# Kernel tuning notes

Measured on AMD Instinct MI355X. Metric: run time of the kernel, lower is better.

The kernel has to match this reference:

```python
import jax, jax.numpy as jnp
import numpy as np

C = 1024
D = C // 8      # query/key channels
R = C // 16     # channel-attention reduction
B, H, W = 4, 64, 64


def setup_inputs() -> dict:
    key = jax.random.key(0)
    ks = jax.random.split(key, 10)
    s = lambda k, shp, fan: jax.random.normal(k, shp, jnp.float32) * (1.0 / np.sqrt(fan))
    return {
        "x": jax.random.normal(ks[0], (B, C, H, W), jnp.float32),
        "x1": jax.random.normal(ks[1], (B, C, H, W), jnp.float32),
        "Wq": s(ks[2], (D, C), C), "bq": jnp.zeros((D,), jnp.float32),
        "Wk": s(ks[3], (D, C), C), "bk": jnp.zeros((D,), jnp.float32),
        "Wv": s(ks[4], (C, C), C), "bv": jnp.zeros((C,), jnp.float32),
        "Wca1": s(ks[5], (R, C), C),  # CBAM MLP, no bias
        "Wca2": s(ks[6], (C, R), R),
    }


def _forward(x, x1, Wq, bq, Wk, bk, Wv, bv, Wca1, Wca2):
    b, c, h, w = x.shape
    n = h * w
    # 1x1 convs as channel matmuls
    Q = (jnp.einsum('bchw,dc->bdhw', x, Wq) + bq[:, None, None]).reshape(b, D, n)   # [B,D,N]
    K = (jnp.einsum('bchw,dc->bdhw', x, Wk) + bk[:, None, None]).reshape(b, D, n)   # [B,D,N]
    V = (jnp.einsum('bchw,oc->bohw', x1, Wv) + bv[:, None, None]).reshape(b, c, n)  # [B,C,N]
    # energy[b,n,m] = Q[:,n] . K[:,m]
    energy = jnp.einsum('bdn,bdm->bnm', Q, K)
    att = jax.nn.sigmoid(energy)                       # [B,N,N]
    # torch: bmm(V, att^T) -> out[b,c,n] = sum_m V[b,c,m] * att[b,n,m]
    out = jnp.einsum('bcm,bnm->bcn', V, att).reshape(b, c, h, w)
    # ChannelAttention (CBAM): shared MLP on avg+max pooled features, sigmoid gate
    avg = out.mean(axis=(2, 3))                        # [B,C]
    mx = out.max(axis=(2, 3))                          # [B,C]
    mlp = lambda v: jnp.einsum('cr,br->bc', Wca2, jax.nn.relu(jnp.einsum('rc,bc->br', Wca1, v)))
    gate = jax.nn.sigmoid(mlp(avg) + mlp(mx))          # [B,C]
    return out * gate[:, :, None, None]


def reference(x, x1, Wq, bq, Wk, bk, Wv, bv, Wca1, Wca2):
    return _forward(x, x1, Wq, bq, Wk, bk, Wv, bv, Wca1, Wca2)
```

## Files before the change

### kernel.cpp

```cpp
#include <hip/hip_runtime.h>
#include <hip/hip_fp16.h>
#include <cstdint>

typedef _Float16 f16;
typedef __attribute__((ext_vector_type(8))) _Float16 half8;
typedef __attribute__((ext_vector_type(16))) float floatx16;

#define CC 1024
#define DD 128
#define RRR 64
#define BBATCH 4
#define NNN 4096

#define BM 128
#define BN 128
#define BK 64

__device__ __forceinline__ void gl_lds16(const void* g, void* l) {
  __builtin_amdgcn_global_load_lds(
      (__attribute__((address_space(1))) void*)(uintptr_t)g,
      (__attribute__((address_space(3))) void*)l, 16, 0, 0);
}

template<int EPI>
__global__ __launch_bounds__(256)
void gemm_bt(const f16* __restrict__ A, const f16* __restrict__ Bp, f16* __restrict__ Cout,
             const float* __restrict__ bias, int N, int K,
             int lda, int ldb, int ldc, size_t sA, size_t sB, size_t sC)
{
  __shared__ __align__(16) f16 S[2 * BM * BK];
  f16* As = S;
  f16* Bs = S + BM * BK;

  const int z = blockIdx.z;
  const int tid  = threadIdx.x;
  const int lane = tid & 63;
  const int wave = tid >> 6;
  const int m0 = blockIdx.y * BM;
  const int n0 = blockIdx.x * BN;
  const int wm = (wave >> 1) * 64;
  const int wn = (wave & 1) * 64;
  const int l31 = lane & 31;
  const int hi  = lane >> 5;
  const int rs  = lane & 7;

  const f16* Ab = A  + (size_t)z * sA + (size_t)m0 * lda;
  const f16* Bb = Bp + (size_t)z * sB + (size_t)n0 * ldb;

  floatx16 acc[2][2];
#pragma unroll
  for (int i = 0; i < 2; ++i)
#pragma unroll
    for (int j = 0; j < 2; ++j)
#pragma unroll
      for (int r = 0; r < 16; ++r)
        acc[i][j][r] = 0.f;

  int srow[4], ssrc[4];
#pragma unroll
  for (int r = 0; r < 4; ++r) {
    const int gi = r * 256 + tid;
    const int row = gi >> 3;
    const int gc  = gi & 7;
    srow[r] = row;
    ssrc[r] = ((gc ^ (row & 7)) << 3);
  }

  for (int k0 = 0; k0 < K; k0 += BK) {
#pragma unroll
    for (int r = 0; r < 4; ++r) {
      gl_lds16(Ab + (size_t)srow[r] * lda + k0 + ssrc[r], As + (size_t)(r * 256 + tid) * 8);
      gl_lds16(Bb + (size_t)srow[r] * ldb + k0 + ssrc[r], Bs + (size_t)(r * 256 + tid) * 8);
    }
    __syncthreads();

#pragma unroll
    for (int kk = 0; kk < BK; kk += 16) {
      const int gr = (((kk >> 3) + hi) ^ rs) << 3;
      half8 af[2], bfr[2];
#pragma unroll
      for (int i = 0; i < 2; ++i)
        af[i] = *(const half8*)(As + (wm + i * 32 + l31) * BK + gr);
#pragma unroll
      for (int j = 0; j < 2; ++j)
        bfr[j] = *(const half8*)(Bs + (wn + j * 32 + l31) * BK + gr);
#pragma unroll
      for (int i = 0; i < 2; ++i)
#pragma unroll
        for (int j = 0; j < 2; ++j)
          acc[i][j] = __builtin_amdgcn_mfma_f32_32x32x16_f16(af[i], bfr[j], acc[i][j], 0, 0, 0);
    }
    __syncthreads();
  }

  f16* Ch = Cout + (size_t)z * sC;
  f16* Ct = S;
#pragma unroll
  for (int i = 0; i < 2; ++i)
#pragma unroll
    for (int j = 0; j < 2; ++j)
#pragma unroll
      for (int r = 0; r < 16; ++r) {
        const int rl = wm + i * 32 + (r & 3) + 8 * (r >> 2) + 4 * hi;
        const int cl = wn + j * 32 + l31;
        const float v = acc[i][j][r];
        f16 h;
        if constexpr (EPI == 0)      h = (f16)v;
        else if constexpr (EPI == 1) h = (f16)(v + bias[m0 + rl]);
        else if constexpr (EPI == 2) h = (f16)(v + bias[n0 + cl]);
        else                         h = (f16)(1.0f / (1.0f + __expf(-v)));
        Ct[rl * BN + ((((cl >> 3) ^ (rl & 7)) << 3) | (cl & 7))] = h;
      }
  __syncthreads();
#pragma unroll
  for (int p = 0; p < 8; ++p) {
    const int idx = p * 256 + tid;
    const int rl = idx >> 4;
    const int g  = idx & 15;
    half8 vv = *(const half8*)(Ct + rl * BN + ((g ^ (rl & 7)) << 3));
    *(half8*)(Ch + (size_t)(m0 + rl) * ldc + n0 + g * 8) = vv;
  }
}

#define G8_STAGE(MATG, MIDX, LD, H, KT, BUF) do {                                   \
    gl_lds16(MATG + (size_t)((H) * 128 + srow) * (LD) + (KT) * 64 + soff,           \
             &S[BUF][MIDX][(H) * 8192 + tid * 8]);                                  \
    gl_lds16(MATG + (size_t)((H) * 128 + 64 + srow) * (LD) + (KT) * 64 + soff,      \
             &S[BUF][MIDX][(H) * 8192 + 4096 + tid * 8]);                           \
  } while (0)

#define G8_LOADA(QM) do {                                                           \
    _Pragma("unroll") for (int mt = 0; mt < 2; ++mt)                                \
    _Pragma("unroll") for (int ks = 0; ks < 4; ++ks)                                \
      af[mt * 4 + ks] = *(const half8*)(Ac + aRow + ((QM) * 2 + mt) * 2048 + sws[ks]); \
  } while (0)

#define G8_LOADB(NT2) do {                                                          \
    _Pragma("unroll") for (int ks = 0; ks < 4; ++ks)                                \
      bf[(NT2) * 4 + ks] = *(const half8*)(Bc + bRow + (NT2) * 2048 + sws[ks]);     \
  } while (0)

#define G8_MFMA(QM, QN) do {                                                        \
    __builtin_amdgcn_s_setprio(1);                                                  \
    _Pragma("unroll") for (int mt = 0; mt < 2; ++mt)                                \
    _Pragma("unroll") for (int ks = 0; ks < 4; ++ks)                                \
      acc[(QM) * 2 + mt][QN] = __builtin_amdgcn_mfma_f32_32x32x16_f16(              \
          af[mt * 4 + ks], bf[(QN) * 4 + ks], acc[(QM) * 2 + mt][QN], 0, 0, 0);     \
    __builtin_amdgcn_s_setprio(0);                                                  \
  } while (0)

template<int EPI>
__global__ __launch_bounds__(512, 2)
void gemm8p(const f16* __restrict__ A, const f16* __restrict__ Bp, f16* __restrict__ Cout,
            const float* __restrict__ bias, int K,
            int lda, int ldb, int ldc, size_t sA, size_t sB, size_t sC)
{
  __shared__ __align__(16) f16 S[2][2][16384];

  const int tid  = threadIdx.x;
  const int lane = tid & 63;
  const int wave = tid >> 6;
  const int wm   = wave >> 2;
  const int wn   = wave & 3;
  const int l31  = lane & 31;
  const int hi   = lane >> 5;
  const int z    = blockIdx.z;
  const int m0   = blockIdx.y * 256;
  const int n0   = blockIdx.x * 256;

  const f16* Ag = A  + (size_t)z * sA + (size_t)m0 * lda;
  const f16* Bg = Bp + (size_t)z * sB + (size_t)n0 * ldb;

  const int srow = tid >> 3;
  const int soff = (((tid & 7) ^ (srow & 7)) << 3);

  int sws[4];
#pragma unroll
  for (int ks = 0; ks < 4; ++ks) sws[ks] = (((ks * 2 + hi) ^ (l31 & 7)) << 3);
  const int aRow = (wm * 128 + l31) * 64;
  const int bRow = (wn * 64 + l31) * 64;

  floatx16 acc[4][2];
#pragma unroll
  for (int i = 0; i < 4; ++i)
#pragma unroll
    for (int j = 0; j < 2; ++j)
#pragma unroll
      for (int r = 0; r < 16; ++r) acc[i][j][r] = 0.f;

  half8 af[8], bf[8];

  G8_STAGE(Ag, 0, lda, 0, 0, 0);
  G8_STAGE(Bg, 1, ldb, 0, 0, 0);
  G8_STAGE(Ag, 0, lda, 1, 0, 0);
  G8_STAGE(Bg, 1, ldb, 1, 0, 0);

  const int NT = K >> 6;
  for (int t = 0; t < NT; ++t) {
    const int cur = t & 1, nxt = cur ^ 1;
    const f16* Ac = &S[cur][0][0];
    const f16* Bc = &S[cur][1][0];
    const bool pf = (t + 1 < NT);

    if (pf) {
      G8_STAGE(Ag, 0, lda, 0, t + 1, nxt);
      G8_STAGE(Bg, 1, ldb, 0, t + 1, nxt);
      asm volatile("s_waitcnt vmcnt(4)" ::: "memory");
    } else {
      asm volatile("s_waitcnt vmcnt(0)" ::: "memory");
    }
    __builtin_amdgcn_s_barrier();
    G8_LOADA(0); G8_LOADB(0);
    asm volatile("s_waitcnt lgkmcnt(0)" ::: "memory");
    __builtin_amdgcn_sched_barrier(0);
    G8_MFMA(0, 0);
    __builtin_amdgcn_s_barrier();

    G8_LOADB(1);
    if (pf) G8_STAGE(Ag, 0, lda, 1, t + 1, nxt);
    __builtin_amdgcn_s_barrier();
    asm volatile("s_waitcnt lgkmcnt(0)" ::: "memory");
    __builtin_amdgcn_sched_barrier(0);
    G8_MFMA(0, 1);
    __builtin_amdgcn_s_barrier();

    G8_LOADA(1);
    if (pf) G8_STAGE(Bg, 1, ldb, 1, t + 1, nxt);
    __builtin_amdgcn_s_barrier();
    asm volatile("s_waitcnt lgkmcnt(0)" ::: "memory");
    __builtin_amdgcn_sched_barrier(0);
    G8_MFMA(1, 1);
    __builtin_amdgcn_s_barrier();

    G8_MFMA(1, 0);
    __builtin_amdgcn_s_barrier();
  }

  f16* Ct = &S[0][0][0];
  f16* Ch = Cout + (size_t)z * sC;
#pragma unroll
  for (int i = 0; i < 4; ++i)
#pragma unroll
    for (int j = 0; j < 2; ++j)
#pragma unroll
      for (int r = 0; r < 16; ++r) {
        const int rl = wm * 128 + i * 32 + (r & 3) + 8 * (r >> 2) + 4 * hi;
        const int cl = wn * 64 + j * 32 + l31;
        const float v = acc[i][j][r];
        f16 h;
        if constexpr (EPI == 1) h = (f16)(v + bias[m0 + rl]);
        else                    h = (f16)v;
        Ct[rl * 256 + ((((cl >> 3) ^ (rl & 7)) << 3) | (cl & 7))] = h;
      }
  asm volatile("s_waitcnt lgkmcnt(0)" ::: "memory");
  __builtin_amdgcn_s_barrier();
#pragma unroll
  for (int p = 0; p < 16; ++p) {
    const int idx = p * 512 + tid;
    const int rl = idx >> 5;
    const int g  = idx & 31;
    half8 vv = *(const half8*)(Ct + rl * 256 + ((g ^ (rl & 7)) << 3));
    *(half8*)(Ch + (size_t)(m0 + rl) * ldc + n0 + g * 8) = vv;
  }
}

#undef G8_STAGE
#undef G8_LOADA
#undef G8_LOADB
#undef G8_MFMA

__global__ __launch_bounds__(256)
void prep(const float* __restrict__ Wq, const float* __restrict__ Wk, const float* __restrict__ Wv,
          const float* __restrict__ bq, const float* __restrict__ bk,
          f16* __restrict__ WQKb, f16* __restrict__ Wvb, float* __restrict__ bqk)
{
  const int NV = CC * CC;
  const int NQ = DD * CC;
  int i = blockIdx.x * 256 + threadIdx.x;
  if (i < NV)                    Wvb[i] = (f16)Wv[i];
  else if (i < NV + NQ)          WQKb[i - NV] = (f16)Wq[i - NV];
  else if (i < NV + 2 * NQ)      WQKb[i - NV] = (f16)Wk[i - NV - NQ];
  else if (i < NV + 2 * NQ + 2 * DD) {
    int t = i - NV - 2 * NQ;
    bqk[t] = (t < DD) ? bq[t] : bk[t - DD];
  }
}

__global__ __launch_bounds__(256)
void transpose_cvt(const float* __restrict__ x, const float* __restrict__ x1,
                   f16* __restrict__ ox, f16* __restrict__ ox1, int nb)
{
  const int zz = blockIdx.z;
  const int b  = (zz < nb) ? zz : zz - nb;
  const float* in = ((zz < nb) ? x : x1) + (size_t)b * CC * NNN;
  f16* out = ((zz < nb) ? ox : ox1) + (size_t)b * CC * NNN;
  __shared__ float tile[64][65];
  const int c0 = blockIdx.y * 64;
  const int n0 = blockIdx.x * 64;
  const int t  = threadIdx.x;
  const int rn = (t & 15) * 4;
  const int rc = t >> 4;
#pragma unroll
  for (int r = 0; r < 4; ++r) {
    const float4 v = *(const float4*)(in + (size_t)(c0 + rc + r * 16) * NNN + n0 + rn);
    tile[rc + r * 16][rn]     = v.x;
    tile[rc + r * 16][rn + 1] = v.y;
    tile[rc + r * 16][rn + 2] = v.z;
    tile[rc + r * 16][rn + 3] = v.w;
  }
  __syncthreads();
  const int ce = (t & 7) * 8;
  const int nr = t >> 3;
#pragma unroll
  for (int r = 0; r < 2; ++r) {
    half8 vv;
#pragma unroll
    for (int e = 0; e < 8; ++e) vv[e] = (f16)tile[ce + e][nr + r * 32];
    *(half8*)(out + (size_t)(n0 + nr + r * 32) * CC + c0 + ce) = vv;
  }
}

__global__ __launch_bounds__(256)
void rowreduce(const f16* __restrict__ X, float* __restrict__ avg, float* __restrict__ mx, int ncols)
{
  const size_t ridx = (size_t)blockIdx.y * gridDim.x + blockIdx.x;
  const half8* p = (const half8*)(X + ridx * ncols);
  float s = 0.f, m = -3.402823466e38f;
  for (int i = threadIdx.x; i < ncols / 8; i += 256) {
    half8 v = p[i];
#pragma unroll
    for (int e = 0; e < 8; ++e) {
      float f = (float)v[e];
      s += f;
      m = fmaxf(m, f);
    }
  }
#pragma unroll
  for (int o = 32; o > 0; o >>= 1) {
    s += __shfl_down(s, o);
    m = fmaxf(m, __shfl_down(m, o));
  }
  __shared__ float ss[4], sm[4];
  if ((threadIdx.x & 63) == 0) { ss[threadIdx.x >> 6] = s; sm[threadIdx.x >> 6] = m; }
  __syncthreads();
  if (threadIdx.x == 0) {
    s = ss[0] + ss[1] + ss[2] + ss[3];
    m = fmaxf(fmaxf(sm[0], sm[1]), fmaxf(sm[2], sm[3]));
    avg[ridx] = s / (float)ncols;
    mx[ridx] = m;
  }
}

__global__ __launch_bounds__(256)
void mlp_gate(const float* __restrict__ avg, const float* __restrict__ mxv,
              const float* __restrict__ W1, const float* __restrict__ W2,
              float* __restrict__ gate)
{
  const int z = blockIdx.x;
  avg += (size_t)z * CC; mxv += (size_t)z * CC; gate += (size_t)z * CC;
  const int t = threadIdx.x;
  const int r = t & 63;
  const int part = t >> 6;
  __shared__ float pa[4][64], pm[4][64], h[RRR];
  {
    const float* w = W1 + (size_t)r * CC + part * 256;
    const float* av = avg + part * 256;
    const float* mv = mxv + part * 256;
    float sa = 0.f, sm = 0.f;
    for (int c = 0; c < 256; ++c) { float wv = w[c]; sa += wv * av[c]; sm += wv * mv[c]; }
    pa[part][r] = sa; pm[part][r] = sm;
  }
  __syncthreads();
  if (t < RRR) {
    float A_ = pa[0][t] + pa[1][t] + pa[2][t] + pa[3][t];
    float M_ = pm[0][t] + pm[1][t] + pm[2][t] + pm[3][t];
    h[t] = fmaxf(A_, 0.f) + fmaxf(M_, 0.f);
  }
  __syncthreads();
  for (int c = t; c < CC; c += 256) {
    float s = 0.f;
    for (int rr = 0; rr < RRR; ++rr) s += W2[(size_t)c * RRR + rr] * h[rr];
    gate[c] = 1.0f / (1.0f + __expf(-s));
  }
}

__global__ __launch_bounds__(256)
void scale_out(const f16* __restrict__ oh, float* __restrict__ out, const float* __restrict__ gate)
{
  oh  += (size_t)blockIdx.y * CC * NNN;
  out += (size_t)blockIdx.y * CC * NNN;
  gate += (size_t)blockIdx.y * CC;
  size_t i = (size_t)blockIdx.x * 256 + threadIdx.x;
  half8 v = ((const half8*)oh)[i];
  const float g = gate[(i * 8) >> 12];
  float4 a = { (float)v[0] * g, (float)v[1] * g, (float)v[2] * g, (float)v[3] * g };
  float4 b = { (float)v[4] * g, (float)v[5] * g, (float)v[6] * g, (float)v[7] * g };
  float4* o = (float4*)out;
  o[2 * i]     = a;
  o[2 * i + 1] = b;
}

extern "C" void kernel_launch(void* const* d_in, const int* in_sizes, int n_in,
                              void* d_out, int out_size, void* d_ws, size_t ws_size,
                              hipStream_t stream)
{
  const float* x    = (const float*)d_in[0];
  const float* x1   = (const float*)d_in[1];
  const float* Wq   = (const float*)d_in[2];
  const float* bq   = (const float*)d_in[3];
  const float* Wk   = (const float*)d_in[4];
  const float* bk   = (const float*)d_in[5];
  const float* Wv   = (const float*)d_in[6];
  const float* bv   = (const float*)d_in[7];
  const float* Wca1 = (const float*)d_in[8];
  const float* Wca2 = (const float*)d_in[9];
  float* out = (float*)d_out;

  char* ws = (char*)d_ws;
  size_t off = 0;
  auto alloc = [&](size_t bytes) { void* p = ws + off; off += (bytes + 255) & ~255ULL; return p; };

  f16* WQKb = (f16*)alloc((size_t)2 * DD * CC * 2);
  f16* Wvb  = (f16*)alloc((size_t)CC * CC * 2);
  float* bqk  = (float*)alloc(256 * 4);
  float* avg  = (float*)alloc((size_t)BBATCH * CC * 4);
  float* mxv  = (float*)alloc((size_t)BBATCH * CC * 4);
  float* gate = (float*)alloc((size_t)BBATCH * CC * 4);

  const size_t attB = (size_t)NNN * NNN * 2;
  const size_t xTB  = (size_t)BBATCH * NNN * CC * 2;
  const size_t qkB  = (size_t)BBATCH * NNN * 2 * DD * 2;
  const size_t vBB  = (size_t)BBATCH * CC * NNN * 2;
  const size_t ohB  = (size_t)BBATCH * CC * NNN * 2;
  const size_t fixedEnd = off;

  const dim3 blk(256);
  const int prepN = CC * CC + 2 * DD * CC + 2 * DD;
  prep<<<(prepN + 255) / 256, blk, 0, stream>>>(Wq, Wk, Wv, bq, bk, WQKb, Wvb, bqk);

  {
    size_t offF = fixedEnd;
    auto af_ = [&](size_t bytes) { void* p = ws + offF; offF += (bytes + 255) & ~255ULL; return p; };
    f16* QKt  = (f16*)af_(qkB);
    f16* Vb   = (f16*)af_(vBB);
    f16* outh = (f16*)af_(ohB);
    f16* att  = (f16*)af_((size_t)BBATCH * attB);
    if (offF + (1 << 20) <= ws_size) {
      f16* xTb  = att;
      f16* x1Tb = att + (size_t)BBATCH * NNN * CC;

      transpose_cvt<<<dim3(NNN / 64, CC / 64, 2 * BBATCH), blk, 0, stream>>>(x, x1, xTb, x1Tb, BBATCH);

      gemm_bt<2><<<dim3(2 * DD / BN, NNN / BM, BBATCH), blk, 0, stream>>>(
          xTb, WQKb, QKt, bqk, 2 * DD, CC,
          CC, CC, 2 * DD, (size_t)NNN * CC, 0, (size_t)NNN * 2 * DD);
      gemm8p<1><<<dim3(NNN / 256, CC / 256, BBATCH), dim3(512), 0, stream>>>(
          Wvb, x1Tb, Vb, bv, CC,
          CC, CC, NNN, 0, (size_t)NNN * CC, (size_t)CC * NNN);

      const size_t sQK = (size_t)NNN * 2 * DD;
      gemm_bt<3><<<dim3(NNN / BN, NNN / BM, BBATCH), blk, 0, stream>>>(
          QKt, QKt + DD, att, nullptr, NNN, DD,
          2 * DD, 2 * DD, NNN, sQK, sQK, (size_t)NNN * NNN);
      gemm8p<0><<<dim3(NNN / 256, CC / 256, BBATCH), dim3(512), 0, stream>>>(
          Vb, att, outh, nullptr, NNN,
          NNN, NNN, NNN, (size_t)CC * NNN, (size_t)NNN * NNN, (size_t)CC * NNN);

      rowreduce<<<dim3(CC, BBATCH), blk, 0, stream>>>(outh, avg, mxv, NNN);
      mlp_gate<<<BBATCH, blk, 0, stream>>>(avg, mxv, Wca1, Wca2, gate);
      scale_out<<<dim3(CC * NNN / 8 / 256, BBATCH), blk, 0, stream>>>(outh, out, gate);
      return;
    }
  }

  int g = 0;
  for (int cand = BBATCH; cand >= 1; cand >>= 1) {
    size_t need = fixedEnd + 2 * xTB + qkB + vBB + ohB + (size_t)cand * attB + (1 << 20);
    if (need <= ws_size) { g = cand; break; }
  }

  if (g > 0) {
    f16* xTb  = (f16*)alloc(xTB);
    f16* x1Tb = (f16*)alloc(xTB);
    f16* QKt  = (f16*)alloc(qkB);
    f16* Vb   = (f16*)alloc(vBB);
    f16* outh = (f16*)alloc(ohB);
    f16* att  = (f16*)alloc((size_t)g * attB);

    transpose_cvt<<<dim3(NNN / 64, CC / 64, 2 * BBATCH), blk, 0, stream>>>(x, x1, xTb, x1Tb, BBATCH);

    gemm_bt<2><<<dim3(2 * DD / BN, NNN / BM, BBATCH), blk, 0, stream>>>(
        xTb, WQKb, QKt, bqk, 2 * DD, CC,
        CC, CC, 2 * DD, (size_t)NNN * CC, 0, (size_t)NNN * 2 * DD);
    gemm_bt<1><<<dim3(NNN / BN, CC / BM, BBATCH), blk, 0, stream>>>(
        Wvb, x1Tb, Vb, bv, NNN, CC,
        CC, CC, NNN, 0, (size_t)NNN * CC, (size_t)CC * NNN);

    for (int b0 = 0; b0 < BBATCH; b0 += g) {
      const int gc = (b0 + g <= BBATCH) ? g : (BBATCH - b0);
      const size_t sQK = (size_t)NNN * 2 * DD;
      gemm_bt<3><<<dim3(NNN / BN, NNN / BM, gc), blk, 0, stream>>>(
          QKt + (size_t)b0 * sQK, QKt + (size_t)b0 * sQK + DD, att, nullptr,
          NNN, DD, 2 * DD, 2 * DD, NNN, sQK, sQK, (size_t)NNN * NNN);
      gemm_bt<0><<<dim3(NNN / BN, CC / BM, gc), blk, 0, stream>>>(
          Vb + (size_t)b0 * CC * NNN, att, outh + (size_t)b0 * CC * NNN, nullptr,
          NNN, NNN, NNN, NNN, NNN,
          (size_t)CC * NNN, (size_t)NNN * NNN, (size_t)CC * NNN);
    }

    rowreduce<<<dim3(CC, BBATCH), blk, 0, stream>>>(outh, avg, mxv, NNN);
    mlp_gate<<<BBATCH, blk, 0, stream>>>(avg, mxv, Wca1, Wca2, gate);
    scale_out<<<dim3(CC * NNN / 8 / 256, BBATCH), blk, 0, stream>>>(outh, out, gate);
  } else {
    f16* xTb  = (f16*)alloc((size_t)NNN * CC * 2);
    f16* x1Tb = (f16*)alloc((size_t)NNN * CC * 2);
    f16* QKt  = (f16*)alloc((size_t)NNN * 2 * DD * 2);
    f16* Vb   = (f16*)alloc((size_t)CC * NNN * 2);
    f16* outh = (f16*)alloc((size_t)CC * NNN * 2);
    f16* att  = (f16*)alloc(attB);

    for (int b = 0; b < BBATCH; ++b) {
      const float* xb  = x  + (size_t)b * CC * NNN;
      const float* x1b = x1 + (size_t)b * CC * NNN;
      float* outb = out + (size_t)b * CC * NNN;

      transpose_cvt<<<dim3(NNN / 64, CC / 64, 2), blk, 0, stream>>>(xb, x1b, xTb, x1Tb, 1);

      gemm_bt<2><<<dim3(2 * DD / BN, NNN / BM, 1), blk, 0, stream>>>(
          xTb, WQKb, QKt, bqk, 2 * DD, CC, CC, CC, 2 * DD, 0, 0, 0);
      gemm_bt<1><<<dim3(NNN / BN, CC / BM, 1), blk, 0, stream>>>(
          Wvb, x1Tb, Vb, bv, NNN, CC, CC, CC, NNN, 0, 0, 0);
      gemm_bt<3><<<dim3(NNN / BN, NNN / BM, 1), blk, 0, stream>>>(
          QKt, QKt + DD, att, nullptr, NNN, DD, 2 * DD, 2 * DD, NNN, 0, 0, 0);
      gemm_bt<0><<<dim3(NNN / BN, CC / BM, 1), blk, 0, stream>>>(
          Vb, att, outh, nullptr, NNN, NNN, NNN, NNN, NNN, 0, 0, 0);

      rowreduce<<<dim3(CC, 1), blk, 0, stream>>>(outh, avg + (size_t)b * CC, mxv + (size_t)b * CC, NNN);
      mlp_gate<<<1, blk, 0, stream>>>(avg + (size_t)b * CC, mxv + (size_t)b * CC, Wca1, Wca2, gate + (size_t)b * CC);
      scale_out<<<dim3(CC * NNN / 8 / 256, 1), blk, 0, stream>>>(outh, outb, gate + (size_t)b * CC);
    }
  }
}
```

Before: 483.7 us.

## Switch gemm8p to 16x16x32 MFMA and use it for the energy GEMM

Rewrites the 256x256 gemm8p kernel to use 16x16x32 f16 MFMA tiles with an 8x4 accumulator grid instead of 32x32x16 tiles. All four next-stage global-to-LDS loads are issued at the top of each K iteration, rather than being spread across the MFMA phases. A sigmoid epilogue (EPI==3) is added, and the QK^T energy GEMM now runs through gemm8p instead of the smaller gemm_bt kernel. This aims to speed up the attention-energy GEMM with the larger tile and the pipelined kernel. The risks are different LDS access patterns, a changed prefetch overlap, and a short K=128 loop for that GEMM.

```diff
diff --git a/kernel.cpp b/kernel.cpp
--- a/kernel.cpp
+++ b/kernel.cpp
@@ -4,6 +4,7 @@
 
 typedef _Float16 f16;
 typedef __attribute__((ext_vector_type(8))) _Float16 half8;
+typedef __attribute__((ext_vector_type(4))) float floatx4;
 typedef __attribute__((ext_vector_type(16))) float floatx16;
 
 #define CC 1024
@@ -129,23 +130,25 @@
              &S[BUF][MIDX][(H) * 8192 + 4096 + tid * 8]);                           \
   } while (0)
 
-#define G8_LOADA(QM) do {                                                           \
-    _Pragma("unroll") for (int mt = 0; mt < 2; ++mt)                                \
-    _Pragma("unroll") for (int ks = 0; ks < 4; ++ks)                                \
-      af[mt * 4 + ks] = *(const half8*)(Ac + aRow + ((QM) * 2 + mt) * 2048 + sws[ks]); \
+#define G8_LDA(MA) do {                                                             \
+    _Pragma("unroll") for (int ms = 0; ms < 4; ++ms)                                \
+    _Pragma("unroll") for (int ks = 0; ks < 2; ++ks)                                \
+      af[ms * 2 + ks] = *(const half8*)(Ac + aRow + (MA) * 4096 + ms * 1024 + sws[ks]); \
   } while (0)
 
-#define G8_LOADB(NT2) do {                                                          \
-    _Pragma("unroll") for (int ks = 0; ks < 4; ++ks)                                \
-      bf[(NT2) * 4 + ks] = *(const half8*)(Bc + bRow + (NT2) * 2048 + sws[ks]);     \
+#define G8_LDB(NH) do {                                                             \
+    _Pragma("unroll") for (int ns = 0; ns < 2; ++ns)                                \
+    _Pragma("unroll") for (int ks = 0; ks < 2; ++ks)                                \
+      bf[NH][ns * 2 + ks] = *(const half8*)(Bc + bRow + (NH) * 2048 + ns * 1024 + sws[ks]); \
   } while (0)
 
-#define G8_MFMA(QM, QN) do {                                                        \
+#define G8_MFMA(MA, NH) do {                                                        \
     __builtin_amdgcn_s_setprio(1);                                                  \
-    _Pragma("unroll") for (int mt = 0; mt < 2; ++mt)                                \
-    _Pragma("unroll") for (int ks = 0; ks < 4; ++ks)                                \
-      acc[(QM) * 2 + mt][QN] = __builtin_amdgcn_mfma_f32_32x32x16_f16(              \
-          af[mt * 4 + ks], bf[(QN) * 4 + ks], acc[(QM) * 2 + mt][QN], 0, 0, 0);     \
+    _Pragma("unroll") for (int ms = 0; ms < 4; ++ms)                                \
+    _Pragma("unroll") for (int ns = 0; ns < 2; ++ns)                                \
+    _Pragma("unroll") for (int ks = 0; ks < 2; ++ks)                                \
+      acc[(MA) * 4 + ms][(NH) * 2 + ns] = __builtin_amdgcn_mfma_f32_16x16x32_f16(   \
+          af[ms * 2 + ks], bf[NH][ns * 2 + ks], acc[(MA) * 4 + ms][(NH) * 2 + ns], 0, 0, 0); \
     __builtin_amdgcn_s_setprio(0);                                                  \
   } while (0)
 
@@ -162,8 +165,8 @@
   const int wave = tid >> 6;
   const int wm   = wave >> 2;
   const int wn   = wave & 3;
-  const int l31  = lane & 31;
-  const int hi   = lane >> 5;
+  const int l15  = lane & 15;
+  const int lk   = lane >> 4;
   const int z    = blockIdx.z;
   const int m0   = blockIdx.y * 256;
   const int n0   = blockIdx.x * 256;
@@ -174,21 +177,21 @@
   const int srow = tid >> 3;
   const int soff = (((tid & 7) ^ (srow & 7)) << 3);
 
-  int sws[4];
-#pragma unroll
-  for (int ks = 0; ks < 4; ++ks) sws[ks] = (((ks * 2 + hi) ^ (l31 & 7)) << 3);
-  const int aRow = (wm * 128 + l31) * 64;
-  const int bRow = (wn * 64 + l31) * 64;
-
-  floatx16 acc[4][2];
-#pragma unroll
-  for (int i = 0; i < 4; ++i)
-#pragma unroll
-    for (int j = 0; j < 2; ++j)
-#pragma unroll
-      for (int r = 0; r < 16; ++r) acc[i][j][r] = 0.f;
-
-  half8 af[8], bf[8];
+  int sws[2];
+#pragma unroll
+  for (int ks = 0; ks < 2; ++ks) sws[ks] = (((ks * 4 + lk) ^ (l15 & 7)) << 3);
+  const int aRow = (wm * 128 + l15) * 64;
+  const int bRow = (wn * 64 + l15) * 64;
+
+  floatx4 acc[8][4];
+#pragma unroll
+  for (int i = 0; i < 8; ++i)
+#pragma unroll
+    for (int j = 0; j < 4; ++j)
+#pragma unroll
+      for (int r = 0; r < 4; ++r) acc[i][j][r] = 0.f;
+
+  half8 af[8], bf[2][4];
 
   G8_STAGE(Ag, 0, lda, 0, 0, 0);
   G8_STAGE(Bg, 1, ldb, 0, 0, 0);
@@ -200,32 +203,31 @@
     const int cur = t & 1, nxt = cur ^ 1;
     const f16* Ac = &S[cur][0][0];
     const f16* Bc = &S[cur][1][0];
-    const bool pf = (t + 1 < NT);
-
-    if (pf) {
+
+    if (t + 1 < NT) {
       G8_STAGE(Ag, 0, lda, 0, t + 1, nxt);
       G8_STAGE(Bg, 1, ldb, 0, t + 1, nxt);
-      asm volatile("s_waitcnt vmcnt(4)" ::: "memory");
+      G8_STAGE(Ag, 0, lda, 1, t + 1, nxt);
+      G8_STAGE(Bg, 1, ldb, 1, t + 1, nxt);
+      asm volatile("s_waitcnt vmcnt(8)" ::: "memory");
     } else {
       asm volatile("s_waitcnt vmcnt(0)" ::: "memory");
     }
     __builtin_amdgcn_s_barrier();
-    G8_LOADA(0); G8_LOADB(0);
+    G8_LDA(0); G8_LDB(0);
     asm volatile("s_waitcnt lgkmcnt(0)" ::: "memory");
     __builtin_amdgcn_sched_barrier(0);
     G8_MFMA(0, 0);
     __builtin_amdgcn_s_barrier();
 
-    G8_LOADB(1);
-    if (pf) G8_STAGE(Ag, 0, lda, 1, t + 1, nxt);
+    G8_LDB(1);
     __builtin_amdgcn_s_barrier();
     asm volatile("s_waitcnt lgkmcnt(0)" ::: "memory");
     __builtin_amdgcn_sched_barrier(0);
     G8_MFMA(0, 1);
     __builtin_amdgcn_s_barrier();
 
-    G8_LOADA(1);
-    if (pf) G8_STAGE(Bg, 1, ldb, 1, t + 1, nxt);
+    G8_LDA(1);
     __builtin_amdgcn_s_barrier();
     asm volatile("s_waitcnt lgkmcnt(0)" ::: "memory");
     __builtin_amdgcn_sched_barrier(0);
@@ -239,17 +241,18 @@
   f16* Ct = &S[0][0][0];
   f16* Ch = Cout + (size_t)z * sC;
 #pragma unroll
-  for (int i = 0; i < 4; ++i)
-#pragma unroll
-    for (int j = 0; j < 2; ++j)
-#pragma unroll
-      for (int r = 0; r < 16; ++r) {
-        const int rl = wm * 128 + i * 32 + (r & 3) + 8 * (r >> 2) + 4 * hi;
-        const int cl = wn * 64 + j * 32 + l31;
-        const float v = acc[i][j][r];
+  for (int mi = 0; mi < 8; ++mi)
+#pragma unroll
+    for (int ni = 0; ni < 4; ++ni)
+#pragma unroll
+      for (int r = 0; r < 4; ++r) {
+        const int rl = wm * 128 + mi * 16 + lk * 4 + r;
+        const int cl = wn * 64 + ni * 16 + l15;
+        const float v = acc[mi][ni][r];
         f16 h;
-        if constexpr (EPI == 1) h = (f16)(v + bias[m0 + rl]);
-        else                    h = (f16)v;
+        if constexpr (EPI == 1)      h = (f16)(v + bias[m0 + rl]);
+        else if constexpr (EPI == 3) h = (f16)(1.0f / (1.0f + __expf(-v)));
+        else                         h = (f16)v;
         Ct[rl * 256 + ((((cl >> 3) ^ (rl & 7)) << 3) | (cl & 7))] = h;
       }
   asm volatile("s_waitcnt lgkmcnt(0)" ::: "memory");
@@ -265,8 +268,8 @@
 }
 
 #undef G8_STAGE
-#undef G8_LOADA
-#undef G8_LOADB
+#undef G8_LDA
+#undef G8_LDB
 #undef G8_MFMA
 
 __global__ __launch_bounds__(256)
@@ -459,8 +462,8 @@
           CC, CC, NNN, 0, (size_t)NNN * CC, (size_t)CC * NNN);
 
       const size_t sQK = (size_t)NNN * 2 * DD;
-      gemm_bt<3><<<dim3(NNN / BN, NNN / BM, BBATCH), blk, 0, stream>>>(
-          QKt, QKt + DD, att, nullptr, NNN, DD,
+      gemm8p<3><<<dim3(NNN / 256, NNN / 256, BBATCH), dim3(512), 0, stream>>>(
+          QKt, QKt + DD, att, nullptr, DD,
           2 * DD, 2 * DD, NNN, sQK, sQK, (size_t)NNN * NNN);
       gemm8p<0><<<dim3(NNN / 256, CC / 256, BBATCH), dim3(512), 0, stream>>>(
           Vb, att, outh, nullptr, NNN,
```

Result: no change. 481.9 us (-0.4%).
